# Kernel tuning notes

Hardware: AMD Instinct MI355X
Metric: run time of the kernel (lower is better)

Reference implementation:

```python
import jax, jax.numpy as jnp
import numpy as np

F_DIM = 1024
D = F_DIM // 2          # trunk width (divisor=2)
T = 1024                # contextlen
B = 32
PI = 256
VF = 256
N_HEADS = 4
EPS = 1e-5


def _posenc(seq_len, d):
    pos = jnp.arange(seq_len, dtype=jnp.float32)[:, None]
    div = jnp.exp(jnp.arange(0, d, 2, dtype=jnp.float32) * (-np.log(10000.0) / d))
    pe = jnp.zeros((seq_len, d), dtype=jnp.float32)
    pe = pe.at[:, 0::2].set(jnp.sin(pos * div))
    pe = pe.at[:, 1::2].set(jnp.cos(pos * div))
    return pe


def _ln(x, g, b):
    mu = x.mean(-1, keepdims=True)
    var = ((x - mu) ** 2).mean(-1, keepdims=True)
    return (x - mu) / jnp.sqrt(var + EPS) * g + b


def setup_inputs() -> dict:
    key = jax.random.key(0)
    ks = iter(jax.random.split(key, 40))
    w = lambda shape: jax.random.normal(next(ks), shape, dtype=jnp.float32) * 0.02
    inp = {
        "features": jax.random.normal(next(ks), (B, T, F_DIM), dtype=jnp.float32),
        "enc_w1": w((F_DIM, D)), "enc_b1": jnp.zeros((D,), jnp.float32),
        "enc_w2": w((D, D)),     "enc_b2": jnp.zeros((D,), jnp.float32),
        "qkv_w": w((D, 3 * D)),  "qkv_b": jnp.zeros((3 * D,), jnp.float32),
        "lam": jnp.float32(0.8),
        "out_w": w((D, D)),      "out_b": jnp.zeros((D,), jnp.float32),
        "ln1_g": jnp.ones((D,), jnp.float32), "ln1_b": jnp.zeros((D,), jnp.float32),
        "ffn_w1": w((D, F_DIM)), "ffn_b1": jnp.zeros((F_DIM,), jnp.float32),
        "ffn_w2": w((F_DIM, D)), "ffn_b2": jnp.zeros((D,), jnp.float32),
        "ln2_g": jnp.ones((D,), jnp.float32), "ln2_b": jnp.zeros((D,), jnp.float32),
        "act_w1": w((D, F_DIM)),       "act_b1": jnp.zeros((F_DIM,), jnp.float32),
        "act_w2": w((F_DIM, 2 * F_DIM)), "act_b2": jnp.zeros((2 * F_DIM,), jnp.float32),
        "act_w3": w((2 * F_DIM, PI)),  "act_b3": jnp.zeros((PI,), jnp.float32),
        "cr_w1": w((D, F_DIM)),        "cr_b1": jnp.zeros((F_DIM,), jnp.float32),
        "cr_w2": w((F_DIM, 2 * F_DIM)), "cr_b2": jnp.zeros((2 * F_DIM,), jnp.float32),
        "cr_w3": w((2 * F_DIM, VF)),   "cr_b3": jnp.zeros((VF,), jnp.float32),
    }
    return inp


def reference(features, enc_w1, enc_b1, enc_w2, enc_b2, qkv_w, qkv_b, lam,
              out_w, out_b, ln1_g, ln1_b, ffn_w1, ffn_b1, ffn_w2, ffn_b2,
              ln2_g, ln2_b, act_w1, act_b1, act_w2, act_b2, act_w3, act_b3,
              cr_w1, cr_b1, cr_w2, cr_b2, cr_w3, cr_b3):
    b, t, f = features.shape
    # encoder MLP: feature_dim -> d -> d with ReLU
    y = jax.nn.relu(features @ enc_w1 + enc_b1)
    y = jax.nn.relu(y @ enc_w2 + enc_b2)            # (B,T,D)
    d = y.shape[-1]
    y = y + _posenc(t, d)
    # differential dual-softmax attention (no head split; head_dim only scales)
    qkv = y @ qkv_w + qkv_b
    q, k, v = jnp.split(qkv, 3, axis=-1)
    q1, q2 = jnp.split(q, 2, axis=-1)
    k1, k2 = jnp.split(k, 2, axis=-1)
    scale = 1.0 / np.sqrt(d // N_HEADS)
    a1 = jax.nn.softmax(jnp.einsum('btc,bsc->bts', q1, k1) * scale, axis=-1)
    a2 = jax.nn.softmax(jnp.einsum('btc,bsc->bts', q2, k2) * scale, axis=-1)
    diff = a1 - lam * a2
    attn = jnp.einsum('bts,bsd->btd', diff, v)      # (B,T,D)
    # faithful to torch: transpose(0,1).contiguous().view(B,-1,D)
    attn = jnp.swapaxes(attn, 0, 1).reshape(b, t, d)
    attn = attn @ out_w + out_b
    y = _ln(y + attn, ln1_g, ln1_b)
    z = jax.nn.relu(y @ ffn_w1 + ffn_b1) @ ffn_w2 + ffn_b2
    y = _ln(y + z, ln2_g, ln2_b)                     # (B,T,D)
    # actor / critic heads, then take last timestep
    a = jax.nn.relu(y @ act_w1 + act_b1)
    a = jax.nn.relu(a @ act_w2 + act_b2)
    a = a @ act_w3 + act_b3
    c = jax.nn.relu(y @ cr_w1 + cr_b1)
    c = jax.nn.relu(c @ cr_w2 + cr_b2)
    c = c @ cr_w3 + cr_b3
    return (a[:, -1, :], c[:, -1, :])
```

## Files before the change

kernel.cpp:

```cpp
#include <hip/hip_runtime.h>
#include <hip/hip_bf16.h>
#include <math.h>

#define TDIM 1024
#define FDIM 1024
#define DDIM 512

typedef __attribute__((ext_vector_type(8))) short bf16x8;
typedef __attribute__((ext_vector_type(8))) ushort u16x8;
typedef __attribute__((ext_vector_type(4))) float f32x4;

__device__ __forceinline__ float posenc_val(int t, int c) {
    int j = c >> 1;
    float dv = expf(-9.210340371976184f * (float)(2 * j) * (1.0f / 512.0f));
    float arg = (float)t * dv;
    return (c & 1) ? cosf(arg) : sinf(arg);
}

__device__ __forceinline__ ushort f2bf(float f) {
    __hip_bfloat16 h = __float2bfloat16(f);
    return *reinterpret_cast<ushort*>(&h);
}

template<int BK>
__device__ __forceinline__ void g32_body(
    const float* X, long lda,
    const float* Pin, int KCx, const float* xbias, int xrelu,
    const float* W, long ldb,
    float* Pout, int N, int K,
    int bx, int by, float* lds)
{
    float (*Xs)[BK + 4] = (float (*)[BK + 4])lds;
    float (*Ws)[64]     = (float (*)[64])(lds + 32 * (BK + 4));
    const int tid = threadIdx.x;
    const int n0 = bx * 64, k0 = by * BK;

    {
        const int m  = tid >> 3;
        const int ks = (tid & 7) * (BK / 8);
        if (Pin) {
            #pragma unroll
            for (int j = 0; j < BK / 32; ++j) {
                float4 a = make_float4(0.f, 0.f, 0.f, 0.f);
                for (int c = 0; c < KCx; ++c) {
                    float4 v = *(const float4*)(Pin + (size_t)(c * 32 + m) * K + k0 + ks + j * 4);
                    a.x += v.x; a.y += v.y; a.z += v.z; a.w += v.w;
                }
                if (xbias) {
                    float4 bv = *(const float4*)(xbias + k0 + ks + j * 4);
                    a.x += bv.x; a.y += bv.y; a.z += bv.z; a.w += bv.w;
                }
                if (xrelu) {
                    a.x = fmaxf(a.x, 0.f); a.y = fmaxf(a.y, 0.f);
                    a.z = fmaxf(a.z, 0.f); a.w = fmaxf(a.w, 0.f);
                }
                *(float4*)&Xs[m][ks + j * 4] = a;
            }
        } else {
            const float* src = X + (size_t)m * lda + k0 + ks;
            #pragma unroll
            for (int j = 0; j < BK / 32; ++j)
                *(float4*)&Xs[m][ks + j * 4] = *(const float4*)(src + j * 4);
        }
    }
    #pragma unroll
    for (int it = 0; it < BK / 16; ++it) {
        int e4  = it * 256 + tid;
        int row = e4 >> 4;
        int c4  = e4 & 15;
        *(float4*)&Ws[row][c4 * 4] = *(const float4*)(W + (size_t)(k0 + row) * ldb + n0 + c4 * 4);
    }
    __syncthreads();

    const int tx = tid & 31;
    const int ty = tid >> 5;
    float acc[4][2] = {};
    #pragma unroll 8
    for (int k = 0; k < BK; k += 4) {
        float4 xv[4];
        #pragma unroll
        for (int i = 0; i < 4; ++i) xv[i] = *(const float4*)&Xs[ty * 4 + i][k];
        #pragma unroll
        for (int j = 0; j < 4; ++j) {
            float2 w = *(const float2*)&Ws[k + j][tx * 2];
            #pragma unroll
            for (int i = 0; i < 4; ++i) {
                float x = ((const float*)&xv[i])[j];
                acc[i][0] = fmaf(x, w.x, acc[i][0]);
                acc[i][1] = fmaf(x, w.y, acc[i][1]);
            }
        }
    }
    float* dst = Pout + (size_t)by * 32 * N;
    #pragma unroll
    for (int i = 0; i < 4; ++i)
        *(float2*)(dst + (size_t)(ty * 4 + i) * N + n0 + tx * 2) = make_float2(acc[i][0], acc[i][1]);
}

template<int BK>
__global__ __launch_bounds__(256) void g32k(
    const float* X0, const float* X1, long lda,
    const float* Pin0, const float* Pin1, int KCx,
    const float* xb0, const float* xb1, int xrelu,
    const float* W0, const float* W1, long ldb,
    float* Pout, int N, int K)
{
    __shared__ __align__(16) float lds[32 * (BK + 4) + BK * 64];
    const int z = blockIdx.z;
    g32_body<BK>(z ? X1 : X0, lda, z ? Pin1 : Pin0, KCx, z ? xb1 : xb0, xrelu,
                 z ? W1 : W0, ldb,
                 Pout + (size_t)z * gridDim.y * 32 * N,
                 N, K, blockIdx.x, blockIdx.y, lds);
}

__device__ __forceinline__ void convT_body(const float* W, int ldw, int col0,
                                           ushort* Wt, int K, int bx, int by, float* lds)
{
    float (*t)[33] = (float (*)[33])lds;
    const int k0 = by * 32, n0 = bx * 32;
    const int x = threadIdx.x & 31, y = threadIdx.x >> 5;
    #pragma unroll
    for (int yy = y; yy < 32; yy += 8)
        t[yy][x] = W[(size_t)(k0 + yy) * ldw + col0 + n0 + x];
    __syncthreads();
    #pragma unroll
    for (int yy = y; yy < 32; yy += 8)
        Wt[(size_t)(n0 + yy) * K + k0 + x] = f2bf(t[x][yy]);
}

__device__ __forceinline__ void mfma_body(
    const void* Aptr, int af32, long lda,
    const ushort* Bt, const float* bias,
    float* C, int ldc, ushort* Cbf, int ldcb,
    int K, int relu, int addpe,
    int bx, int by, char* smem)
{
    ushort* Al = (ushort*)smem;
    ushort* Bl = Al + 64 * 64;
    const int tid = threadIdx.x;
    const int m0 = by * 64;
    const int n0 = bx * 64;
    const int lane = tid & 63;
    const int wv = tid >> 6;
    const int wr = wv >> 1, wc = wv & 1;
    const int fr = lane & 15, g = lane >> 4;

    f32x4 acc[2][2] = {};

    const int r0 = tid >> 3;
    const int c0 = tid & 7;

    for (int k0 = 0; k0 < K; k0 += 64) {
        #pragma unroll
        for (int it = 0; it < 2; ++it) {
            int r = r0 + it * 32;
            if (af32) {
                const float* Af = (const float*)Aptr;
                const float* s = Af + (size_t)(m0 + r) * lda + k0 + c0 * 8;
                float4 u = *(const float4*)s;
                float4 v = *(const float4*)(s + 4);
                u16x8 pv;
                pv[0] = f2bf(u.x); pv[1] = f2bf(u.y); pv[2] = f2bf(u.z); pv[3] = f2bf(u.w);
                pv[4] = f2bf(v.x); pv[5] = f2bf(v.y); pv[6] = f2bf(v.z); pv[7] = f2bf(v.w);
                *(u16x8*)((char*)Al + r * 128 + ((c0 ^ (r & 7)) << 4)) = pv;
            } else {
                const ushort* Au = (const ushort*)Aptr;
                uint4 va = *(const uint4*)(Au + (size_t)(m0 + r) * lda + k0 + c0 * 8);
                *(uint4*)((char*)Al + r * 128 + ((c0 ^ (r & 7)) << 4)) = va;
            }
            uint4 vb = *(const uint4*)(Bt + (size_t)(n0 + r) * K + k0 + c0 * 8);
            *(uint4*)((char*)Bl + r * 128 + ((c0 ^ (r & 7)) << 4)) = vb;
        }
        __syncthreads();
        #pragma unroll
        for (int h = 0; h < 2; ++h) {
            bf16x8 af[2], bff[2];
            #pragma unroll
            for (int i = 0; i < 2; ++i) {
                int row = wr * 32 + i * 16 + fr;
                af[i] = *(const bf16x8*)((const char*)Al + row * 128 + (((h * 4 + g) ^ (row & 7)) << 4));
                int col = wc * 32 + i * 16 + fr;
                bff[i] = *(const bf16x8*)((const char*)Bl + col * 128 + (((h * 4 + g) ^ (col & 7)) << 4));
            }
            #pragma unroll
            for (int i = 0; i < 2; ++i)
                #pragma unroll
                for (int j = 0; j < 2; ++j)
                    acc[i][j] = __builtin_amdgcn_mfma_f32_16x16x32_bf16(af[i], bff[j], acc[i][j], 0, 0, 0);
        }
        __syncthreads();
    }

    #pragma unroll
    for (int j = 0; j < 2; ++j) {
        int n = n0 + wc * 32 + j * 16 + fr;
        float bv = bias ? bias[n] : 0.f;
        #pragma unroll
        for (int i = 0; i < 2; ++i) {
            #pragma unroll
            for (int q = 0; q < 4; ++q) {
                int m = m0 + wr * 32 + i * 16 + g * 4 + q;
                float v = acc[i][j][q] + bv;
                if (relu) v = fmaxf(v, 0.f);
                if (addpe) v += posenc_val(m, n);
                if (C)   C[(size_t)m * ldc + n] = v;
                if (Cbf) Cbf[(size_t)m * ldcb + n] = f2bf(v);
            }
        }
    }
}

__global__ __launch_bounds__(256) void mfma_k(
    const void* A, int af32, long lda, const ushort* Bt, const float* bias,
    float* C, int ldc, ushort* Cbf, int ldcb, int K, int relu, int pe)
{
    __shared__ __align__(16) char smem[16384];
    mfma_body(A, af32, lda, Bt, bias, C, ldc, Cbf, ldcb, K, relu, pe,
              blockIdx.x, blockIdx.y, smem);
}

__global__ __launch_bounds__(256) void prep_k(
    const float* features, const float* enc_w1, const float* qkv_w, const float* enc_w2,
    ushort* w1T, ushort* w2T, ushort* qkvT, float* P_enc1)
{
    __shared__ __align__(16) float lds[6272];
    int t = blockIdx.x;
    if (t < 128) {
        g32_body<64>(features + (size_t)1023 * FDIM, (long)TDIM * FDIM,
                     nullptr, 0, nullptr, 0,
                     enc_w1, DDIM, P_enc1, 512, 1024, t & 7, t >> 3, lds);
    } else if (t < 640) {
        int u = t - 128;
        convT_body(enc_w1, 512, 0, w1T, 1024, u & 15, u >> 4, lds);
    } else if (t < 896) {
        int u = t - 640;
        convT_body(enc_w2, 512, 0, w2T, 512, u & 15, u >> 4, lds);
    } else {
        int u = t - 896;
        convT_body(qkv_w, 1536, 0, qkvT, 512, u % 48, u / 48, lds);
    }
}

__global__ __launch_bounds__(256) void stage2_k(
    const float* features31, const ushort* w1T, const float* enc_b1, ushort* H1bf,
    const float* P_enc1, const float* enc_w2, float* P_enc2)
{
    __shared__ __align__(16) char smem[25600];
    int t = blockIdx.x;
    if (t < 128) {
        mfma_body(features31, 1, 1024, w1T, enc_b1, nullptr, 0, H1bf, 512,
                  1024, 1, 0, t & 7, t >> 3, smem);
    } else {
        int u = t - 128;
        g32_body<64>(nullptr, 0, P_enc1, 16, enc_b1, 1,
                     enc_w2, 512, P_enc2, 512, 512, u & 7, u >> 3, (float*)smem);
    }
}

__device__ void scores_body(const float* QKV, float* Psc, int bxs, int byc, char* smem)
{
    float (*Kt)[132] = (float (*)[132])smem;
    float (*Qt)[133] = (float (*)[133])(smem + 64 * 132 * 4);
    const int tid = threadIdx.x;
    const int s0 = bxs * 64;
    const int k0 = byc * 128;

    #pragma unroll
    for (int it = 0; it < 8; ++it) {
        int e4 = it * 256 + tid;
        int r  = e4 >> 5;
        int c4 = e4 & 31;
        float4 v = *(const float4*)(QKV + (size_t)(s0 + r) * 1536 + 512 + k0 + c4 * 4);
        *(float4*)&Kt[r][c4 * 4] = v;
    }
    #pragma unroll
    for (int it = 0; it < 4; ++it) {
        int e4 = it * 256 + tid;
        int r  = e4 >> 5;
        int c4 = e4 & 31;
        float4 v = *(const float4*)(QKV + (size_t)(32 * r + 31) * 1536 + k0 + c4 * 4);
        Qt[r][c4 * 4 + 0] = v.x;
        Qt[r][c4 * 4 + 1] = v.y;
        Qt[r][c4 * 4 + 2] = v.z;
        Qt[r][c4 * 4 + 3] = v.w;
    }
    __syncthreads();

    const int i  = tid & 31;
    const int sg = tid >> 5;
    float acc[8] = {};
    for (int k = 0; k < 128; ++k) {
        float q = Qt[i][k];
        #pragma unroll
        for (int j = 0; j < 8; ++j)
            acc[j] = fmaf(Kt[sg * 8 + j][k], q, acc[j]);
    }
    float* dst = Psc + (size_t)byc * 1024 * 32;
    #pragma unroll
    for (int j = 0; j < 8; ++j)
        dst[(size_t)(s0 + sg * 8 + j) * 32 + i] = acc[j];
}

__global__ __launch_bounds__(256) void stage5_k(
    const float* QKV, float* Psc,
    const float* P_enc2, const float* enc_b2, float* ylast)
{
    __shared__ __align__(16) char smem[50816];
    int t = blockIdx.x;
    if (t < 64) {
        scores_body(QKV, Psc, t & 15, t >> 4, smem);
    } else {
        int blk = t - 64;
        for (int idx = threadIdx.x; idx < 4 * 512; idx += 256) {
            int r = idx >> 9, c = idx & 511;
            int m = blk * 4 + r;
            float s = enc_b2[c];
            for (int cc = 0; cc < 8; ++cc) s += P_enc2[(size_t)(cc * 32 + m) * 512 + c];
            s = fmaxf(s, 0.f) + posenc_val(1023, c);
            ylast[m * 512 + c] = s;
        }
    }
}

__global__ __launch_bounds__(256) void softmax_diff(
    const float* __restrict__ Psc, const float* __restrict__ lam_p, float* __restrict__ D)
{
    __shared__ float sc1[TDIM];
    __shared__ float sc2[TDIM];
    __shared__ float red[256];
    const int i = blockIdx.x;
    const int tid = threadIdx.x;
    const float scale = 0.08838834764831845f;
    for (int s = tid; s < TDIM; s += 256) {
        float a = Psc[(size_t)(0 * 1024 + s) * 32 + i] + Psc[(size_t)(1 * 1024 + s) * 32 + i];
        float b = Psc[(size_t)(2 * 1024 + s) * 32 + i] + Psc[(size_t)(3 * 1024 + s) * 32 + i];
        sc1[s] = a * scale;
        sc2[s] = b * scale;
    }
    __syncthreads();
    float m1 = -INFINITY, m2 = -INFINITY;
    for (int s = tid; s < TDIM; s += 256) { m1 = fmaxf(m1, sc1[s]); m2 = fmaxf(m2, sc2[s]); }
    red[tid] = m1; __syncthreads();
    for (int o = 128; o > 0; o >>= 1) { if (tid < o) red[tid] = fmaxf(red[tid], red[tid + o]); __syncthreads(); }
    m1 = red[0]; __syncthreads();
    red[tid] = m2; __syncthreads();
    for (int o = 128; o > 0; o >>= 1) { if (tid < o) red[tid] = fmaxf(red[tid], red[tid + o]); __syncthreads(); }
    m2 = red[0]; __syncthreads();
    float t1 = 0.f, t2 = 0.f;
    for (int s = tid; s < TDIM; s += 256) { t1 += expf(sc1[s] - m1); t2 += expf(sc2[s] - m2); }
    red[tid] = t1; __syncthreads();
    for (int o = 128; o > 0; o >>= 1) { if (tid < o) red[tid] += red[tid + o]; __syncthreads(); }
    t1 = red[0]; __syncthreads();
    red[tid] = t2; __syncthreads();
    for (int o = 128; o > 0; o >>= 1) { if (tid < o) red[tid] += red[tid + o]; __syncthreads(); }
    t2 = red[0]; __syncthreads();
    const float inv1 = 1.f / t1, inv2 = 1.f / t2;
    const float lam = *lam_p;
    for (int s = tid; s < TDIM; s += 256)
        D[(size_t)i * TDIM + s] = expf(sc1[s] - m1) * inv1 - lam * expf(sc2[s] - m2) * inv2;
}

__global__ __launch_bounds__(256) void ln_red(
    const float* __restrict__ Pin, int KC, const float* __restrict__ bias,
    const float* __restrict__ R, const float* __restrict__ g, const float* __restrict__ b,
    float* __restrict__ Y)
{
    __shared__ float red[256];
    const int m = blockIdx.x;
    const int tid = threadIdx.x;
    float v0 = bias ? bias[tid] : 0.f;
    float v1 = bias ? bias[tid + 256] : 0.f;
    for (int c = 0; c < KC; ++c) {
        v0 += Pin[(size_t)(c * 32 + m) * 512 + tid];
        v1 += Pin[(size_t)(c * 32 + m) * 512 + tid + 256];
    }
    v0 += R[m * 512 + tid];
    v1 += R[m * 512 + tid + 256];
    red[tid] = v0 + v1; __syncthreads();
    for (int o = 128; o > 0; o >>= 1) { if (tid < o) red[tid] += red[tid + o]; __syncthreads(); }
    const float mu = red[0] * (1.0f / 512.0f);
    __syncthreads();
    float d0 = v0 - mu, d1 = v1 - mu;
    red[tid] = d0 * d0 + d1 * d1; __syncthreads();
    for (int o = 128; o > 0; o >>= 1) { if (tid < o) red[tid] += red[tid + o]; __syncthreads(); }
    const float var = red[0] * (1.0f / 512.0f);
    const float inv = 1.0f / sqrtf(var + 1e-5f);
    Y[m * 512 + tid]       = d0 * inv * g[tid]       + b[tid];
    Y[m * 512 + 256 + tid] = d1 * inv * g[256 + tid] + b[256 + tid];
}

__global__ __launch_bounds__(256) void fin_out(
    const float* __restrict__ P, const float* __restrict__ b0, const float* __restrict__ b1,
    float* __restrict__ out)
{
    const int m = blockIdx.x;
    const int z = blockIdx.y;
    const int n = threadIdx.x;
    const float* bias = z ? b1 : b0;
    const float* Pz = P + (size_t)z * 16 * 32 * 256;
    float s = bias[n];
    for (int c = 0; c < 16; ++c) s += Pz[(size_t)(c * 32 + m) * 256 + n];
    out[z * 8192 + m * 256 + n] = s;
}

extern "C" void kernel_launch(void* const* d_in, const int* in_sizes, int n_in,
                              void* d_out, int out_size, void* d_ws, size_t ws_size,
                              hipStream_t stream)
{
    const float* features = (const float*)d_in[0];
    const float* enc_w1 = (const float*)d_in[1];
    const float* enc_b1 = (const float*)d_in[2];
    const float* enc_w2 = (const float*)d_in[3];
    const float* enc_b2 = (const float*)d_in[4];
    const float* qkv_w  = (const float*)d_in[5];
    const float* qkv_b  = (const float*)d_in[6];
    const float* lam    = (const float*)d_in[7];
    const float* out_w  = (const float*)d_in[8];
    const float* out_b  = (const float*)d_in[9];
    const float* ln1_g  = (const float*)d_in[10];
    const float* ln1_b  = (const float*)d_in[11];
    const float* ffn_w1 = (const float*)d_in[12];
    const float* ffn_b1 = (const float*)d_in[13];
    const float* ffn_w2 = (const float*)d_in[14];
    const float* ffn_b2 = (const float*)d_in[15];
    const float* ln2_g  = (const float*)d_in[16];
    const float* ln2_b  = (const float*)d_in[17];
    const float* act_w1 = (const float*)d_in[18];
    const float* act_b1 = (const float*)d_in[19];
    const float* act_w2 = (const float*)d_in[20];
    const float* act_b2 = (const float*)d_in[21];
    const float* act_w3 = (const float*)d_in[22];
    const float* act_b3 = (const float*)d_in[23];
    const float* cr_w1  = (const float*)d_in[24];
    const float* cr_b1  = (const float*)d_in[25];
    const float* cr_w2  = (const float*)d_in[26];
    const float* cr_b2  = (const float*)d_in[27];
    const float* cr_w3  = (const float*)d_in[28];
    const float* cr_b3  = (const float*)d_in[29];
    float* out = (float*)d_out;

    char* base = (char*)d_ws;
    ushort* w1T    = (ushort*)(base + 0x000000);
    ushort* w2T    = (ushort*)(base + 0x100000);
    ushort* qkvT   = (ushort*)(base + 0x180000);
    ushort* H1bf   = (ushort*)(base + 0x300000);
    ushort* Y31bf  = (ushort*)(base + 0x400000);
    float*  QKV    = (float*)(base + 0x500000);
    float*  Psc    = (float*)(base + 0xB00000);
    float*  Dbuf   = (float*)(base + 0xB80000);
    float*  ylast  = (float*)(base + 0xBA0000);
    float*  y1     = (float*)(base + 0xBB0000);
    float*  y2     = (float*)(base + 0xBC0000);
    float*  P_enc1 = (float*)(base + 0xC00000);
    float*  P_enc2 = (float*)(base + 0xD00000);
    float*  P_attn = (float*)(base + 0xD80000);
    float*  P_atp  = (float*)(base + 0xE80000);
    float*  P_h    = (float*)(base + 0xF00000);
    float*  P_z    = (float*)(base + 0x1000000);
    float*  P_a1   = (float*)(base + 0x1100000);
    float*  P_a2   = (float*)(base + 0x1300000);
    float*  P_a3   = (float*)(base + 0x1700000);

    const float* features31 = features + (size_t)31 * TDIM * FDIM;
    dim3 blk(256);
    const float* NPF = nullptr;

    prep_k<<<1664, blk, 0, stream>>>(features, enc_w1, qkv_w, enc_w2, w1T, w2T, qkvT, P_enc1);
    stage2_k<<<192, blk, 0, stream>>>(features31, w1T, enc_b1, H1bf, P_enc1, enc_w2, P_enc2);
    mfma_k<<<dim3(8, 16), blk, 0, stream>>>(H1bf, 0, 512, w2T, enc_b2,
                                            nullptr, 0, Y31bf, 512, 512, 1, 1);
    mfma_k<<<dim3(24, 16), blk, 0, stream>>>(Y31bf, 0, 512, qkvT, qkv_b,
                                             QKV, 1536, nullptr, 0, 512, 0, 0);
    stage5_k<<<72, blk, 0, stream>>>(QKV, Psc, P_enc2, enc_b2, ylast);
    softmax_diff<<<32, blk, 0, stream>>>(Psc, lam, Dbuf);
    g32k<64><<<dim3(8, 16, 1), blk, 0, stream>>>(Dbuf, NPF, 1024, NPF, NPF, 0, NPF, NPF, 0,
                                                 QKV + 1024, NPF, 1536, P_attn, 512, 1024);
    g32k<64><<<dim3(8, 8, 1), blk, 0, stream>>>(NPF, NPF, 0, P_attn, NPF, 16, NPF, NPF, 0,
                                                out_w, NPF, 512, P_atp, 512, 512);
    ln_red<<<32, blk, 0, stream>>>(P_atp, 8, out_b, ylast, ln1_g, ln1_b, y1);
    g32k<64><<<dim3(16, 8, 1), blk, 0, stream>>>(y1, NPF, 512, NPF, NPF, 0, NPF, NPF, 0,
                                                 ffn_w1, NPF, 1024, P_h, 1024, 512);
    g32k<64><<<dim3(8, 16, 1), blk, 0, stream>>>(NPF, NPF, 0, P_h, NPF, 8, ffn_b1, NPF, 1,
                                                 ffn_w2, NPF, 512, P_z, 512, 1024);
    ln_red<<<32, blk, 0, stream>>>(P_z, 16, ffn_b2, y1, ln2_g, ln2_b, y2);
    g32k<64><<<dim3(16, 8, 2), blk, 0, stream>>>(y2, y2, 512, NPF, NPF, 0, NPF, NPF, 0,
                                                 act_w1, cr_w1, 1024, P_a1, 1024, 512);
    g32k<128><<<dim3(32, 8, 2), blk, 0, stream>>>(NPF, NPF, 0, P_a1, P_a1 + 8 * 32 * 1024, 8,
                                                  act_b1, cr_b1, 1,
                                                  act_w2, cr_w2, 2048, P_a2, 2048, 1024);
    g32k<128><<<dim3(4, 16, 2), blk, 0, stream>>>(NPF, NPF, 0, P_a2, P_a2 + 8 * 32 * 2048, 8,
                                                  act_b2, cr_b2, 1,
                                                  act_w3, cr_w3, 256, P_a3, 256, 2048);
    fin_out<<<dim3(32, 2), blk, 0, stream>>>(P_a3, act_b3, cr_b3, out);
}
```

Before: 141.6 us.

## Fuse all stages into one cooperative persistent kernel with grid syncs

Replaces the chain of about fifteen separate kernel launches with a single cooperative kernel of 256 blocks. The blocks loop over each stage's work items and separate stages with grid.sync(), which removes per-launch overhead and the gaps between launches. The fp32-to-bf16 conversion of features[31] moves into the prep stage, so the MFMA A-loader becomes bf16-only. In exchange, stages with few work items leave most blocks idle while waiting at barriers, and featbf shares its workspace region with P_a1, which is only safe because of the stage ordering.

```diff
diff --git a/kernel.cpp b/kernel.cpp
--- a/kernel.cpp
+++ b/kernel.cpp
@@ -1,13 +1,15 @@
 #include <hip/hip_runtime.h>
+#include <hip/hip_cooperative_groups.h>
 #include <hip/hip_bf16.h>
 #include <math.h>
+
+namespace cg = cooperative_groups;
 
 #define TDIM 1024
 #define FDIM 1024
 #define DDIM 512
 
 typedef __attribute__((ext_vector_type(8))) short bf16x8;
-typedef __attribute__((ext_vector_type(8))) ushort u16x8;
 typedef __attribute__((ext_vector_type(4))) float f32x4;
 
 __device__ __forceinline__ float posenc_val(int t, int c) {
@@ -97,22 +99,6 @@
         *(float2*)(dst + (size_t)(ty * 4 + i) * N + n0 + tx * 2) = make_float2(acc[i][0], acc[i][1]);
 }
 
-template<int BK>
-__global__ __launch_bounds__(256) void g32k(
-    const float* X0, const float* X1, long lda,
-    const float* Pin0, const float* Pin1, int KCx,
-    const float* xb0, const float* xb1, int xrelu,
-    const float* W0, const float* W1, long ldb,
-    float* Pout, int N, int K)
-{
-    __shared__ __align__(16) float lds[32 * (BK + 4) + BK * 64];
-    const int z = blockIdx.z;
-    g32_body<BK>(z ? X1 : X0, lda, z ? Pin1 : Pin0, KCx, z ? xb1 : xb0, xrelu,
-                 z ? W1 : W0, ldb,
-                 Pout + (size_t)z * gridDim.y * 32 * N,
-                 N, K, blockIdx.x, blockIdx.y, lds);
-}
-
 __device__ __forceinline__ void convT_body(const float* W, int ldw, int col0,
                                            ushort* Wt, int K, int bx, int by, float* lds)
 {
@@ -129,7 +115,7 @@
 }
 
 __device__ __forceinline__ void mfma_body(
-    const void* Aptr, int af32, long lda,
+    const ushort* A, long lda,
     const ushort* Bt, const float* bias,
     float* C, int ldc, ushort* Cbf, int ldcb,
     int K, int relu, int addpe,
@@ -154,20 +140,8 @@
         #pragma unroll
         for (int it = 0; it < 2; ++it) {
             int r = r0 + it * 32;
-            if (af32) {
-                const float* Af = (const float*)Aptr;
-                const float* s = Af + (size_t)(m0 + r) * lda + k0 + c0 * 8;
-                float4 u = *(const float4*)s;
-                float4 v = *(const float4*)(s + 4);
-                u16x8 pv;
-                pv[0] = f2bf(u.x); pv[1] = f2bf(u.y); pv[2] = f2bf(u.z); pv[3] = f2bf(u.w);
-                pv[4] = f2bf(v.x); pv[5] = f2bf(v.y); pv[6] = f2bf(v.z); pv[7] = f2bf(v.w);
-                *(u16x8*)((char*)Al + r * 128 + ((c0 ^ (r & 7)) << 4)) = pv;
-            } else {
-                const ushort* Au = (const ushort*)Aptr;
-                uint4 va = *(const uint4*)(Au + (size_t)(m0 + r) * lda + k0 + c0 * 8);
-                *(uint4*)((char*)Al + r * 128 + ((c0 ^ (r & 7)) << 4)) = va;
-            }
+            uint4 va = *(const uint4*)(A + (size_t)(m0 + r) * lda + k0 + c0 * 8);
+            *(uint4*)((char*)Al + r * 128 + ((c0 ^ (r & 7)) << 4)) = va;
             uint4 vb = *(const uint4*)(Bt + (size_t)(n0 + r) * K + k0 + c0 * 8);
             *(uint4*)((char*)Bl + r * 128 + ((c0 ^ (r & 7)) << 4)) = vb;
         }
@@ -210,54 +184,7 @@
     }
 }
 
-__global__ __launch_bounds__(256) void mfma_k(
-    const void* A, int af32, long lda, const ushort* Bt, const float* bias,
-    float* C, int ldc, ushort* Cbf, int ldcb, int K, int relu, int pe)
-{
-    __shared__ __align__(16) char smem[16384];
-    mfma_body(A, af32, lda, Bt, bias, C, ldc, Cbf, ldcb, K, relu, pe,
-              blockIdx.x, blockIdx.y, smem);
-}
-
-__global__ __launch_bounds__(256) void prep_k(
-    const float* features, const float* enc_w1, const float* qkv_w, const float* enc_w2,
-    ushort* w1T, ushort* w2T, ushort* qkvT, float* P_enc1)
-{
-    __shared__ __align__(16) float lds[6272];
-    int t = blockIdx.x;
-    if (t < 128) {
-        g32_body<64>(features + (size_t)1023 * FDIM, (long)TDIM * FDIM,
-                     nullptr, 0, nullptr, 0,
-                     enc_w1, DDIM, P_enc1, 512, 1024, t & 7, t >> 3, lds);
-    } else if (t < 640) {
-        int u = t - 128;
-        convT_body(enc_w1, 512, 0, w1T, 1024, u & 15, u >> 4, lds);
-    } else if (t < 896) {
-        int u = t - 640;
-        convT_body(enc_w2, 512, 0, w2T, 512, u & 15, u >> 4, lds);
-    } else {
-        int u = t - 896;
-        convT_body(qkv_w, 1536, 0, qkvT, 512, u % 48, u / 48, lds);
-    }
-}
-
-__global__ __launch_bounds__(256) void stage2_k(
-    const float* features31, const ushort* w1T, const float* enc_b1, ushort* H1bf,
-    const float* P_enc1, const float* enc_w2, float* P_enc2)
-{
-    __shared__ __align__(16) char smem[25600];
-    int t = blockIdx.x;
-    if (t < 128) {
-        mfma_body(features31, 1, 1024, w1T, enc_b1, nullptr, 0, H1bf, 512,
-                  1024, 1, 0, t & 7, t >> 3, smem);
-    } else {
-        int u = t - 128;
-        g32_body<64>(nullptr, 0, P_enc1, 16, enc_b1, 1,
-                     enc_w2, 512, P_enc2, 512, 512, u & 7, u >> 3, (float*)smem);
-    }
-}
-
-__device__ void scores_body(const float* QKV, float* Psc, int bxs, int byc, char* smem)
+__device__ __forceinline__ void scores_body(const float* QKV, float* Psc, int bxs, int byc, char* smem)
 {
     float (*Kt)[132] = (float (*)[132])smem;
     float (*Qt)[133] = (float (*)[133])(smem + 64 * 132 * 4);
@@ -301,45 +228,23 @@
         dst[(size_t)(s0 + sg * 8 + j) * 32 + i] = acc[j];
 }
 
-__global__ __launch_bounds__(256) void stage5_k(
-    const float* QKV, float* Psc,
-    const float* P_enc2, const float* enc_b2, float* ylast)
-{
-    __shared__ __align__(16) char smem[50816];
-    int t = blockIdx.x;
-    if (t < 64) {
-        scores_body(QKV, Psc, t & 15, t >> 4, smem);
-    } else {
-        int blk = t - 64;
-        for (int idx = threadIdx.x; idx < 4 * 512; idx += 256) {
-            int r = idx >> 9, c = idx & 511;
-            int m = blk * 4 + r;
-            float s = enc_b2[c];
-            for (int cc = 0; cc < 8; ++cc) s += P_enc2[(size_t)(cc * 32 + m) * 512 + c];
-            s = fmaxf(s, 0.f) + posenc_val(1023, c);
-            ylast[m * 512 + c] = s;
-        }
-    }
-}
-
-__global__ __launch_bounds__(256) void softmax_diff(
-    const float* __restrict__ Psc, const float* __restrict__ lam_p, float* __restrict__ D)
-{
-    __shared__ float sc1[TDIM];
-    __shared__ float sc2[TDIM];
-    __shared__ float red[256];
-    const int i = blockIdx.x;
+__device__ __forceinline__ void softmax_body(const float* Psc, const float* lam_p,
+                                             float* D, int i, float* lds)
+{
+    float* sc1 = lds;
+    float* sc2 = lds + 1024;
+    float* red = lds + 2048;
     const int tid = threadIdx.x;
     const float scale = 0.08838834764831845f;
-    for (int s = tid; s < TDIM; s += 256) {
-        float a = Psc[(size_t)(0 * 1024 + s) * 32 + i] + Psc[(size_t)(1 * 1024 + s) * 32 + i];
-        float b = Psc[(size_t)(2 * 1024 + s) * 32 + i] + Psc[(size_t)(3 * 1024 + s) * 32 + i];
+    for (int s = tid; s < 1024; s += 256) {
+        float a = Psc[(size_t)s * 32 + i] + Psc[(size_t)(1024 + s) * 32 + i];
+        float b = Psc[(size_t)(2048 + s) * 32 + i] + Psc[(size_t)(3072 + s) * 32 + i];
         sc1[s] = a * scale;
         sc2[s] = b * scale;
     }
     __syncthreads();
     float m1 = -INFINITY, m2 = -INFINITY;
-    for (int s = tid; s < TDIM; s += 256) { m1 = fmaxf(m1, sc1[s]); m2 = fmaxf(m2, sc2[s]); }
+    for (int s = tid; s < 1024; s += 256) { m1 = fmaxf(m1, sc1[s]); m2 = fmaxf(m2, sc2[s]); }
     red[tid] = m1; __syncthreads();
     for (int o = 128; o > 0; o >>= 1) { if (tid < o) red[tid] = fmaxf(red[tid], red[tid + o]); __syncthreads(); }
     m1 = red[0]; __syncthreads();
@@ -347,7 +252,7 @@
     for (int o = 128; o > 0; o >>= 1) { if (tid < o) red[tid] = fmaxf(red[tid], red[tid + o]); __syncthreads(); }
     m2 = red[0]; __syncthreads();
     float t1 = 0.f, t2 = 0.f;
-    for (int s = tid; s < TDIM; s += 256) { t1 += expf(sc1[s] - m1); t2 += expf(sc2[s] - m2); }
+    for (int s = tid; s < 1024; s += 256) { t1 += expf(sc1[s] - m1); t2 += expf(sc2[s] - m2); }
     red[tid] = t1; __syncthreads();
     for (int o = 128; o > 0; o >>= 1) { if (tid < o) red[tid] += red[tid + o]; __syncthreads(); }
     t1 = red[0]; __syncthreads();
@@ -356,17 +261,14 @@
     t2 = red[0]; __syncthreads();
     const float inv1 = 1.f / t1, inv2 = 1.f / t2;
     const float lam = *lam_p;
-    for (int s = tid; s < TDIM; s += 256)
-        D[(size_t)i * TDIM + s] = expf(sc1[s] - m1) * inv1 - lam * expf(sc2[s] - m2) * inv2;
-}
-
-__global__ __launch_bounds__(256) void ln_red(
-    const float* __restrict__ Pin, int KC, const float* __restrict__ bias,
-    const float* __restrict__ R, const float* __restrict__ g, const float* __restrict__ b,
-    float* __restrict__ Y)
-{
-    __shared__ float red[256];
-    const int m = blockIdx.x;
+    for (int s = tid; s < 1024; s += 256)
+        D[(size_t)i * 1024 + s] = expf(sc1[s] - m1) * inv1 - lam * expf(sc2[s] - m2) * inv2;
+}
+
+__device__ __forceinline__ void ln_body(const float* Pin, int KC, const float* bias,
+                                        const float* R, const float* g, const float* b,
+                                        float* Y, int m, float* red)
+{
     const int tid = threadIdx.x;
     float v0 = bias ? bias[tid] : 0.f;
     float v1 = bias ? bias[tid + 256] : 0.f;
@@ -389,107 +291,229 @@
     Y[m * 512 + 256 + tid] = d1 * inv * g[256 + tid] + b[256 + tid];
 }
 
-__global__ __launch_bounds__(256) void fin_out(
-    const float* __restrict__ P, const float* __restrict__ b0, const float* __restrict__ b1,
-    float* __restrict__ out)
-{
-    const int m = blockIdx.x;
-    const int z = blockIdx.y;
-    const int n = threadIdx.x;
-    const float* bias = z ? b1 : b0;
-    const float* Pz = P + (size_t)z * 16 * 32 * 256;
-    float s = bias[n];
-    for (int c = 0; c < 16; ++c) s += Pz[(size_t)(c * 32 + m) * 256 + n];
-    out[z * 8192 + m * 256 + n] = s;
+struct KP {
+    const float *features, *enc_w1, *enc_b1, *enc_w2, *enc_b2, *qkv_w, *qkv_b, *lam;
+    const float *out_w, *out_b, *ln1_g, *ln1_b, *ffn_w1, *ffn_b1, *ffn_w2, *ffn_b2;
+    const float *ln2_g, *ln2_b, *act_w1, *act_b1, *act_w2, *act_b2, *act_w3, *act_b3;
+    const float *cr_w1, *cr_b1, *cr_w2, *cr_b2, *cr_w3, *cr_b3;
+    float* out;
+    ushort *w1T, *w2T, *qkvT, *H1bf, *Y31bf, *featbf;
+    float *QKV, *Psc, *Dbuf, *ylast, *y1, *y2;
+    float *P_enc1, *P_enc2, *P_attn, *P_atp, *P_h, *P_z, *P_a1, *P_a2, *P_a3;
+};
+
+__global__ __launch_bounds__(256)
+void mega(KP p)
+{
+    __shared__ __align__(16) char smem[51200];
+    float* lds = (float*)smem;
+    cg::grid_group grid = cg::this_grid();
+    const int nb = gridDim.x;
+
+    for (int u = blockIdx.x; u < 1792; u += nb) {
+        if (u < 128) {
+            g32_body<64>(p.features + (size_t)1023 * FDIM, (long)TDIM * FDIM,
+                         nullptr, 0, nullptr, 0,
+                         p.enc_w1, DDIM, p.P_enc1, 512, 1024, u & 7, u >> 3, lds);
+        } else if (u < 640) {
+            int v = u - 128; convT_body(p.enc_w1, 512, 0, p.w1T, 1024, v & 15, v >> 4, lds);
+        } else if (u < 896) {
+            int v = u - 640; convT_body(p.enc_w2, 512, 0, p.w2T, 512, v & 15, v >> 4, lds);
+        } else if (u < 1664) {
+            int v = u - 896; convT_body(p.qkv_w, 1536, 0, p.qkvT, 512, v % 48, v / 48, lds);
+        } else {
+            int v = u - 1664;
+            const float4* src = (const float4*)(p.features + (size_t)31 * TDIM * FDIM);
+            for (int e = v * 2048 + threadIdx.x; e < v * 2048 + 2048; e += 256) {
+                float4 w = src[e];
+                ushort4 o;
+                o.x = f2bf(w.x); o.y = f2bf(w.y); o.z = f2bf(w.z); o.w = f2bf(w.w);
+                ((ushort4*)p.featbf)[e] = o;
+            }
+        }
+        __syncthreads();
+    }
+    grid.sync();
+
+    for (int u = blockIdx.x; u < 192; u += nb) {
+        if (u < 128)
+            mfma_body(p.featbf, 1024, p.w1T, p.enc_b1, nullptr, 0, p.H1bf, 512,
+                      1024, 1, 0, u & 7, u >> 3, smem);
+        else {
+            int v = u - 128;
+            g32_body<64>(nullptr, 0, p.P_enc1, 16, p.enc_b1, 1,
+                         p.enc_w2, 512, p.P_enc2, 512, 512, v & 7, v >> 3, lds);
+        }
+        __syncthreads();
+    }
+    grid.sync();
+
+    for (int u = blockIdx.x; u < 160; u += nb) {
+        if (u < 128)
+            mfma_body(p.H1bf, 512, p.w2T, p.enc_b2, nullptr, 0, p.Y31bf, 512,
+                      512, 1, 1, u & 7, u >> 3, smem);
+        else {
+            int m = u - 128;
+            #pragma unroll
+            for (int half = 0; half < 2; ++half) {
+                int c = threadIdx.x + half * 256;
+                float s = p.enc_b2[c];
+                for (int cc = 0; cc < 8; ++cc) s += p.P_enc2[(size_t)(cc * 32 + m) * 512 + c];
+                s = fmaxf(s, 0.f) + posenc_val(1023, c);
+                p.ylast[m * 512 + c] = s;
+            }
+        }
+        __syncthreads();
+    }
+    grid.sync();
+
+    for (int u = blockIdx.x; u < 384; u += nb) {
+        mfma_body(p.Y31bf, 512, p.qkvT, p.qkv_b, p.QKV, 1536, nullptr, 0,
+                  512, 0, 0, u % 24, u / 24, smem);
+        __syncthreads();
+    }
+    grid.sync();
+
+    for (int u = blockIdx.x; u < 64; u += nb) {
+        scores_body(p.QKV, p.Psc, u & 15, u >> 4, smem);
+        __syncthreads();
+    }
+    grid.sync();
+
+    for (int u = blockIdx.x; u < 32; u += nb) {
+        softmax_body(p.Psc, p.lam, p.Dbuf, u, lds);
+        __syncthreads();
+    }
+    grid.sync();
+
+    for (int u = blockIdx.x; u < 128; u += nb) {
+        g32_body<64>(p.Dbuf, 1024, nullptr, 0, nullptr, 0,
+                     p.QKV + 1024, 1536, p.P_attn, 512, 1024, u & 7, u >> 3, lds);
+        __syncthreads();
+    }
+    grid.sync();
+
+    for (int u = blockIdx.x; u < 64; u += nb) {
+        g32_body<64>(nullptr, 0, p.P_attn, 16, nullptr, 0,
+                     p.out_w, 512, p.P_atp, 512, 512, u & 7, u >> 3, lds);
+        __syncthreads();
+    }
+    grid.sync();
+
+    for (int u = blockIdx.x; u < 32; u += nb) {
+        ln_body(p.P_atp, 8, p.out_b, p.ylast, p.ln1_g, p.ln1_b, p.y1, u, lds);
+        __syncthreads();
+    }
+    grid.sync();
+
+    for (int u = blockIdx.x; u < 128; u += nb) {
+        g32_body<64>(p.y1, 512, nullptr, 0, nullptr, 0,
+                     p.ffn_w1, 1024, p.P_h, 1024, 512, u & 15, u >> 4, lds);
+        __syncthreads();
+    }
+    grid.sync();
+
+    for (int u = blockIdx.x; u < 128; u += nb) {
+        g32_body<64>(nullptr, 0, p.P_h, 8, p.ffn_b1, 1,
+                     p.ffn_w2, 512, p.P_z, 512, 1024, u & 7, u >> 3, lds);
+        __syncthreads();
+    }
+    grid.sync();
+
+    for (int u = blockIdx.x; u < 32; u += nb) {
+        ln_body(p.P_z, 16, p.ffn_b2, p.y1, p.ln2_g, p.ln2_b, p.y2, u, lds);
+        __syncthreads();
+    }
+    grid.sync();
+
+    for (int u = blockIdx.x; u < 256; u += nb) {
+        int z = u >> 7, v = u & 127;
+        g32_body<64>(p.y2, 512, nullptr, 0, nullptr, 0,
+                     z ? p.cr_w1 : p.act_w1, 1024,
+                     p.P_a1 + (size_t)z * 8 * 32 * 1024, 1024, 512, v & 15, v >> 4, lds);
+        __syncthreads();
+    }
+    grid.sync();
+
+    for (int u = blockIdx.x; u < 512; u += nb) {
+        int z = u >> 8, v = u & 255;
+        g32_body<128>(nullptr, 0, p.P_a1 + (size_t)z * 8 * 32 * 1024, 8,
+                      z ? p.cr_b1 : p.act_b1, 1,
+                      z ? p.cr_w2 : p.act_w2, 2048,
+                      p.P_a2 + (size_t)z * 8 * 32 * 2048, 2048, 1024, v & 31, v >> 5, lds);
+        __syncthreads();
+    }
+    grid.sync();
+
+    for (int u = blockIdx.x; u < 128; u += nb) {
+        int z = u >> 6, v = u & 63;
+        g32_body<128>(nullptr, 0, p.P_a2 + (size_t)z * 8 * 32 * 2048, 8,
+                      z ? p.cr_b2 : p.act_b2, 1,
+                      z ? p.cr_w3 : p.act_w3, 256,
+                      p.P_a3 + (size_t)z * 16 * 32 * 256, 256, 2048, v & 3, v >> 2, lds);
+        __syncthreads();
+    }
+    grid.sync();
+
+    for (int u = blockIdx.x; u < 64; u += nb) {
+        int m = u & 31, z = u >> 5;
+        const float* bias = z ? p.cr_b3 : p.act_b3;
+        const float* Pz = p.P_a3 + (size_t)z * 16 * 32 * 256;
+        int n = threadIdx.x;
+        float s = bias[n];
+        for (int c = 0; c < 16; ++c) s += Pz[(size_t)(c * 32 + m) * 256 + n];
+        p.out[z * 8192 + m * 256 + n] = s;
+        __syncthreads();
+    }
 }
 
 extern "C" void kernel_launch(void* const* d_in, const int* in_sizes, int n_in,
                               void* d_out, int out_size, void* d_ws, size_t ws_size,
                               hipStream_t stream)
 {
-    const float* features = (const float*)d_in[0];
-    const float* enc_w1 = (const float*)d_in[1];
-    const float* enc_b1 = (const float*)d_in[2];
-    const float* enc_w2 = (const float*)d_in[3];
-    const float* enc_b2 = (const float*)d_in[4];
-    const float* qkv_w  = (const float*)d_in[5];
-    const float* qkv_b  = (const float*)d_in[6];
-    const float* lam    = (const float*)d_in[7];
-    const float* out_w  = (const float*)d_in[8];
-    const float* out_b  = (const float*)d_in[9];
-    const float* ln1_g  = (const float*)d_in[10];
-    const float* ln1_b  = (const float*)d_in[11];
-    const float* ffn_w1 = (const float*)d_in[12];
-    const float* ffn_b1 = (const float*)d_in[13];
-    const float* ffn_w2 = (const float*)d_in[14];
-    const float* ffn_b2 = (const float*)d_in[15];
-    const float* ln2_g  = (const float*)d_in[16];
-    const float* ln2_b  = (const float*)d_in[17];
-    const float* act_w1 = (const float*)d_in[18];
-    const float* act_b1 = (const float*)d_in[19];
-    const float* act_w2 = (const float*)d_in[20];
-    const float* act_b2 = (const float*)d_in[21];
-    const float* act_w3 = (const float*)d_in[22];
-    const float* act_b3 = (const float*)d_in[23];
-    const float* cr_w1  = (const float*)d_in[24];
-    const float* cr_b1  = (const float*)d_in[25];
-    const float* cr_w2  = (const float*)d_in[26];
-    const float* cr_b2  = (const float*)d_in[27];
-    const float* cr_w3  = (const float*)d_in[28];
-    const float* cr_b3  = (const float*)d_in[29];
-    float* out = (float*)d_out;
-
     char* base = (char*)d_ws;
-    ushort* w1T    = (ushort*)(base + 0x000000);
-    ushort* w2T    = (ushort*)(base + 0x100000);
-    ushort* qkvT   = (ushort*)(base + 0x180000);
-    ushort* H1bf   = (ushort*)(base + 0x300000);
-    ushort* Y31bf  = (ushort*)(base + 0x400000);
-    float*  QKV    = (float*)(base + 0x500000);
-    float*  Psc    = (float*)(base + 0xB00000);
-    float*  Dbuf   = (float*)(base + 0xB80000);
-    float*  ylast  = (float*)(base + 0xBA0000);
-    float*  y1     = (float*)(base + 0xBB0000);
-    float*  y2     = (float*)(base + 0xBC0000);
-    float*  P_enc1 = (float*)(base + 0xC00000);
-    float*  P_enc2 = (float*)(base + 0xD00000);
-    float*  P_attn = (float*)(base + 0xD80000);
-    float*  P_atp  = (float*)(base + 0xE80000);
-    float*  P_h    = (float*)(base + 0xF00000);
-    float*  P_z    = (float*)(base + 0x1000000);
-    float*  P_a1   = (float*)(base + 0x1100000);
-    float*  P_a2   = (float*)(base + 0x1300000);
-    float*  P_a3   = (float*)(base + 0x1700000);
-
-    const float* features31 = features + (size_t)31 * TDIM * FDIM;
-    dim3 blk(256);
-    const float* NPF = nullptr;
-
-    prep_k<<<1664, blk, 0, stream>>>(features, enc_w1, qkv_w, enc_w2, w1T, w2T, qkvT, P_enc1);
-    stage2_k<<<192, blk, 0, stream>>>(features31, w1T, enc_b1, H1bf, P_enc1, enc_w2, P_enc2);
-    mfma_k<<<dim3(8, 16), blk, 0, stream>>>(H1bf, 0, 512, w2T, enc_b2,
-                                            nullptr, 0, Y31bf, 512, 512, 1, 1);
-    mfma_k<<<dim3(24, 16), blk, 0, stream>>>(Y31bf, 0, 512, qkvT, qkv_b,
-                                             QKV, 1536, nullptr, 0, 512, 0, 0);
-    stage5_k<<<72, blk, 0, stream>>>(QKV, Psc, P_enc2, enc_b2, ylast);
-    softmax_diff<<<32, blk, 0, stream>>>(Psc, lam, Dbuf);
-    g32k<64><<<dim3(8, 16, 1), blk, 0, stream>>>(Dbuf, NPF, 1024, NPF, NPF, 0, NPF, NPF, 0,
-                                                 QKV + 1024, NPF, 1536, P_attn, 512, 1024);
-    g32k<64><<<dim3(8, 8, 1), blk, 0, stream>>>(NPF, NPF, 0, P_attn, NPF, 16, NPF, NPF, 0,
-                                                out_w, NPF, 512, P_atp, 512, 512);
-    ln_red<<<32, blk, 0, stream>>>(P_atp, 8, out_b, ylast, ln1_g, ln1_b, y1);
-    g32k<64><<<dim3(16, 8, 1), blk, 0, stream>>>(y1, NPF, 512, NPF, NPF, 0, NPF, NPF, 0,
-                                                 ffn_w1, NPF, 1024, P_h, 1024, 512);
-    g32k<64><<<dim3(8, 16, 1), blk, 0, stream>>>(NPF, NPF, 0, P_h, NPF, 8, ffn_b1, NPF, 1,
-                                                 ffn_w2, NPF, 512, P_z, 512, 1024);
-    ln_red<<<32, blk, 0, stream>>>(P_z, 16, ffn_b2, y1, ln2_g, ln2_b, y2);
-    g32k<64><<<dim3(16, 8, 2), blk, 0, stream>>>(y2, y2, 512, NPF, NPF, 0, NPF, NPF, 0,
-                                                 act_w1, cr_w1, 1024, P_a1, 1024, 512);
-    g32k<128><<<dim3(32, 8, 2), blk, 0, stream>>>(NPF, NPF, 0, P_a1, P_a1 + 8 * 32 * 1024, 8,
-                                                  act_b1, cr_b1, 1,
-                                                  act_w2, cr_w2, 2048, P_a2, 2048, 1024);
-    g32k<128><<<dim3(4, 16, 2), blk, 0, stream>>>(NPF, NPF, 0, P_a2, P_a2 + 8 * 32 * 2048, 8,
-                                                  act_b2, cr_b2, 1,
-                                                  act_w3, cr_w3, 256, P_a3, 256, 2048);
-    fin_out<<<dim3(32, 2), blk, 0, stream>>>(P_a3, act_b3, cr_b3, out);
-}
+
+    KP p;
+    p.features = (const float*)d_in[0];
+    p.enc_w1 = (const float*)d_in[1];  p.enc_b1 = (const float*)d_in[2];
+    p.enc_w2 = (const float*)d_in[3];  p.enc_b2 = (const float*)d_in[4];
+    p.qkv_w  = (const float*)d_in[5];  p.qkv_b  = (const float*)d_in[6];
+    p.lam    = (const float*)d_in[7];
+    p.out_w  = (const float*)d_in[8];  p.out_b  = (const float*)d_in[9];
+    p.ln1_g  = (const float*)d_in[10]; p.ln1_b  = (const float*)d_in[11];
+    p.ffn_w1 = (const float*)d_in[12]; p.ffn_b1 = (const float*)d_in[13];
+    p.ffn_w2 = (const float*)d_in[14]; p.ffn_b2 = (const float*)d_in[15];
+    p.ln2_g  = (const float*)d_in[16]; p.ln2_b  = (const float*)d_in[17];
+    p.act_w1 = (const float*)d_in[18]; p.act_b1 = (const float*)d_in[19];
+    p.act_w2 = (const float*)d_in[20]; p.act_b2 = (const float*)d_in[21];
+    p.act_w3 = (const float*)d_in[22]; p.act_b3 = (const float*)d_in[23];
+    p.cr_w1  = (const float*)d_in[24]; p.cr_b1  = (const float*)d_in[25];
+    p.cr_w2  = (const float*)d_in[26]; p.cr_b2  = (const float*)d_in[27];
+    p.cr_w3  = (const float*)d_in[28]; p.cr_b3  = (const float*)d_in[29];
+    p.out    = (float*)d_out;
+
+    p.w1T    = (ushort*)(base + 0x000000);
+    p.w2T    = (ushort*)(base + 0x100000);
+    p.qkvT   = (ushort*)(base + 0x180000);
+    p.H1bf   = (ushort*)(base + 0x300000);
+    p.Y31bf  = (ushort*)(base + 0x400000);
+    p.QKV    = (float*)(base + 0x500000);
+    p.Psc    = (float*)(base + 0xB00000);
+    p.Dbuf   = (float*)(base + 0xB80000);
+    p.ylast  = (float*)(base + 0xBA0000);
+    p.y1     = (float*)(base + 0xBB0000);
+    p.y2     = (float*)(base + 0xBC0000);
+    p.P_enc1 = (float*)(base + 0xC00000);
+    p.P_enc2 = (float*)(base + 0xD00000);
+    p.P_attn = (float*)(base + 0xD80000);
+    p.P_atp  = (float*)(base + 0xE80000);
+    p.P_h    = (float*)(base + 0xF00000);
+    p.P_z    = (float*)(base + 0x1000000);
+    p.P_a1   = (float*)(base + 0x1100000);
+    p.P_a2   = (float*)(base + 0x1300000);
+    p.P_a3   = (float*)(base + 0x1700000);
+    p.featbf = (ushort*)(base + 0x1100000);
+
+    void* kargs[] = { (void*)&p };
+    hipLaunchCooperativeKernel((const void*)mega, dim3(256), dim3(256), kargs, 0, stream);
+}
```

Measured after the change: 562.1 us. 297% more time.
